# Performance work log

Hardware: AMD Instinct MI355X
Metric: run time of the kernel (lower is better)

Reference implementation:

```python
import jax, jax.numpy as jnp
import numpy as np

HEADS = 8
DIM_HEAD = 64
SCALE = DIM_HEAD ** -0.5


def setup_inputs() -> dict:
    key = jax.random.key(0)
    k1, k2, k3, k4 = jax.random.split(key, 4)
    dim = 512
    inner = HEADS * DIM_HEAD  # 512
    x = jax.random.normal(k1, (4, 2048, dim), dtype=jnp.float32)
    # torch nn.Linear weight layout: [out_features, in_features]
    w_qkv = jax.random.normal(k2, (inner * 3, dim), dtype=jnp.float32) * (dim ** -0.5)
    w_out = jax.random.normal(k3, (dim, inner), dtype=jnp.float32) * (inner ** -0.5)
    b_out = jax.random.normal(k4, (dim,), dtype=jnp.float32) * 0.01
    return {"x": x, "w_qkv": w_qkv, "w_out": w_out, "b_out": b_out}


def reference(x, w_qkv, w_out, b_out):
    b, n, _ = x.shape
    qkv = x @ w_qkv.T                                   # [b, n, 3*inner]
    q, k, v = jnp.split(qkv, 3, axis=-1)
    def to_heads(t):
        return t.reshape(b, n, HEADS, DIM_HEAD).transpose(0, 2, 1, 3)  # b h n d
    q, k, v = to_heads(q), to_heads(k), to_heads(v)
    dots = jnp.einsum('bhid,bhjd->bhij', q, k) * SCALE  # [b, h, n, n]
    attn = jax.nn.softmax(dots, axis=-1)
    out = jnp.einsum('bhij,bhjd->bhid', attn, v)        # [b, h, n, d]
    out = out.transpose(0, 2, 1, 3).reshape(b, n, HEADS * DIM_HEAD)
    return out @ w_out.T + b_out                        # [b, n, dim]
```

## Files before the change

kernel.cpp:

```cpp
#include <hip/hip_runtime.h>

typedef unsigned int u32;
typedef unsigned short u16;
typedef float f32x4 __attribute__((ext_vector_type(4)));
typedef u32 u32x4 __attribute__((ext_vector_type(4)));
typedef u32 u32x2 __attribute__((ext_vector_type(2)));

__device__ __forceinline__ u16 f2bf(float f) {
    u32 u = __builtin_bit_cast(u32, f);
    u = (u + 0x7FFFu + ((u >> 16) & 1u)) >> 16;
    return (u16)u;
}

__device__ __forceinline__ void mfma16(f32x4& d, const u32x4& a, const u32x4& b) {
    asm("v_mfma_f32_16x16x32_bf16 %0, %1, %2, %0" : "+v"(d) : "v"(a), "v"(b));
}

__device__ __forceinline__ float exp2a(float x) {
    float r;
    asm("v_exp_f32 %0, %1\n\ts_nop 1" : "=v"(r) : "v"(x));
    return r;
}
__device__ __forceinline__ u32 cvtpk(float lo, float hi) {
    u32 r;
    asm("v_cvt_pk_bf16_f32 %0, %1, %2" : "=v"(r) : "v"(lo), "v"(hi));
    return r;
}
__device__ __forceinline__ void gload_lds16(const u16* g, u16* l) {
    __builtin_amdgcn_global_load_lds(
        (const __attribute__((address_space(1))) u32*)g,
        (__attribute__((address_space(3))) u32*)l, 16, 0, 0);
}

__global__ __launch_bounds__(256) void cast3_kernel(
    const float* __restrict__ x, const float* __restrict__ wq,
    const float* __restrict__ wo, u16* __restrict__ xb,
    u16* __restrict__ wqb, u16* __restrict__ wob) {
    int bid = blockIdx.x;
    const float* src;
    u16* dst;
    int base;
    if (bid < 2048)      { src = x;  dst = xb;  base = bid * 2048; }
    else if (bid < 2432) { src = wq; dst = wqb; base = (bid - 2048) * 2048; }
    else                 { src = wo; dst = wob; base = (bid - 2432) * 2048; }
    int i = base + threadIdx.x * 8;
    float4 a = *(const float4*)(src + i);
    float4 b = *(const float4*)(src + i + 4);
    u32x4 r;
    r.x = (u32)f2bf(a.x) | ((u32)f2bf(a.y) << 16);
    r.y = (u32)f2bf(a.z) | ((u32)f2bf(a.w) << 16);
    r.z = (u32)f2bf(b.x) | ((u32)f2bf(b.y) << 16);
    r.w = (u32)f2bf(b.z) | ((u32)f2bf(b.w) << 16);
    *(u32x4*)(dst + i) = r;
}

template <int MODE>
__global__ __launch_bounds__(256) void gemm_bt(
    const u16* __restrict__ A, const u16* __restrict__ B, int K, int N,
    u16* __restrict__ qo, u16* __restrict__ ko, u16* __restrict__ vto,
    float* __restrict__ fo, const float* __restrict__ bias)
{
    __shared__ __align__(16) u16 Al[128 * 64];
    __shared__ __align__(16) u16 Bl[128 * 64];
    const int t = threadIdx.x;
    const int w = t >> 6, l = t & 63;
    const int wr = w >> 1, wc = w & 1;
    const int g = l >> 4, li = l & 15;
    const int m0 = blockIdx.x * 128, n0 = blockIdx.y * 128;

    const f32x4 z = {0.f, 0.f, 0.f, 0.f};
    f32x4 acc[4][4];
#pragma unroll
    for (int mi = 0; mi < 4; ++mi)
#pragma unroll
        for (int ni = 0; ni < 4; ++ni) acc[mi][ni] = z;

    int goff[4], ldst[4];
#pragma unroll
    for (int rnd = 0; rnd < 4; ++rnd) {
        int s = rnd * 256 + t;
        int p = s >> 3, cp = s & 7;
        int cg = cp ^ (p & 7);
        goff[rnd] = p * K + cg * 8;
        ldst[rnd] = s * 8;
    }

    for (int k0 = 0; k0 < K; k0 += 64) {
        __syncthreads();
#pragma unroll
        for (int rnd = 0; rnd < 4; ++rnd) {
            gload_lds16(A + (size_t)m0 * K + k0 + goff[rnd], &Al[ldst[rnd]]);
            gload_lds16(B + (size_t)n0 * K + k0 + goff[rnd], &Bl[ldst[rnd]]);
        }
        __syncthreads();
#pragma unroll
        for (int ks = 0; ks < 2; ++ks) {
            u32x4 af[4], bf[4];
#pragma unroll
            for (int mi = 0; mi < 4; ++mi)
                af[mi] = *(const u32x4*)&Al[(wr * 64 + mi * 16 + li) * 64
                                            + (((ks * 4 + g) ^ (li & 7)) * 8)];
#pragma unroll
            for (int ni = 0; ni < 4; ++ni)
                bf[ni] = *(const u32x4*)&Bl[(wc * 64 + ni * 16 + li) * 64
                                            + (((ks * 4 + g) ^ (li & 7)) * 8)];
#pragma unroll
            for (int mi = 0; mi < 4; ++mi)
#pragma unroll
                for (int ni = 0; ni < 4; ++ni) mfma16(acc[mi][ni], af[mi], bf[ni]);
        }
    }

#pragma unroll
    for (int mi = 0; mi < 4; ++mi) {
#pragma unroll
        for (int ni = 0; ni < 4; ++ni) {
            int o = n0 + wc * 64 + ni * 16 + li;
            int m_base = m0 + wr * 64 + mi * 16 + g * 4;
            if (MODE == 0) {
                int part = o >> 9, oi = o & 511;
                int h = oi >> 6, d = oi & 63;
                int bb = m_base >> 11, nn = m_base & 2047;
                if (part == 2) {
                    u32x2 pv;
                    pv.x = (u32)f2bf(acc[mi][ni][0]) | ((u32)f2bf(acc[mi][ni][1]) << 16);
                    pv.y = (u32)f2bf(acc[mi][ni][2]) | ((u32)f2bf(acc[mi][ni][3]) << 16);
                    *(u32x2*)(vto + ((size_t)(bb * 8 + h) * 64 + d) * 2048 + nn) = pv;
                } else {
                    u16* dst = (part == 0) ? qo : ko;
#pragma unroll
                    for (int r = 0; r < 4; ++r)
                        dst[((size_t)(bb * 8 + h) * 2048 + nn + r) * 64 + d] =
                            f2bf(acc[mi][ni][r]);
                }
            } else {
#pragma unroll
                for (int r = 0; r < 4; ++r)
                    fo[(size_t)(m_base + r) * N + o] = acc[mi][ni][r] + bias[o];
            }
        }
    }
}

__global__ __launch_bounds__(256) void attn_kernel(
    const u16* __restrict__ Q, const u16* __restrict__ Kg,
    const u16* __restrict__ VT, u16* __restrict__ O)
{
    __shared__ __align__(16) u16 Kl[64 * 64];
    __shared__ __align__(16) u16 Vl[64 * 64];
    const int t = threadIdx.x;
    const int w = t >> 6, l = t & 63;
    const int g = l >> 4, li = l & 15;
    const int pair = blockIdx.y;
    const int q0 = blockIdx.x * 128 + w * 32;
    const float CEXP = 0.18033688011112042f;

    u32x4 qf[2][2];
#pragma unroll
    for (int qb = 0; qb < 2; ++qb)
#pragma unroll
        for (int f = 0; f < 2; ++f)
            qf[qb][f] = *(const u32x4*)(Q + ((size_t)pair * 2048 + q0 + qb * 16 + li) * 64
                                          + f * 32 + g * 8);

    const f32x4 z = {0.f, 0.f, 0.f, 0.f};
    f32x4 oacc[2][4];
#pragma unroll
    for (int qb = 0; qb < 2; ++qb)
#pragma unroll
        for (int dc = 0; dc < 4; ++dc) oacc[qb][dc] = z;
    float m_r[2] = {-1e30f, -1e30f};
    float l_r[2] = {0.f, 0.f};

    for (int kt = 0; kt < 32; ++kt) {
        __syncthreads();
#pragma unroll
        for (int i = 0; i < 2; ++i) {
            int s = i * 256 + t;
            int p = s >> 3, cp = s & 7;
            int cg = (cp ^ (p & 7)) * 8;
            int kr = (p & 0x23) | ((p & 0x0C) << 1) | ((p & 0x10) >> 2);
            u32x4 kv = *(const u32x4*)(Kg + ((size_t)pair * 2048 + kt * 64 + kr) * 64 + cg);
            u32x4 vv = *(const u32x4*)(VT + ((size_t)pair * 64 + p) * 2048 + kt * 64 + cg);
            *(u32x4*)&Kl[p * 64 + cp * 8] = kv;
            *(u32x4*)&Vl[p * 64 + cp * 8] = vv;
        }
        __syncthreads();

        f32x4 st[2][4];
#pragma unroll
        for (int qb = 0; qb < 2; ++qb)
#pragma unroll
            for (int kc = 0; kc < 4; ++kc) st[qb][kc] = z;
#pragma unroll
        for (int kc = 0; kc < 4; ++kc)
#pragma unroll
            for (int f = 0; f < 2; ++f) {
                u32x4 kf = *(const u32x4*)&Kl[(kc * 16 + li) * 64
                                              + (((4 * f + g) ^ (li & 7)) * 8)];
                mfma16(st[0][kc], kf, qf[0][f]);
                mfma16(st[1][kc], kf, qf[1][f]);
            }

        u32x4 pb[2][2];
#pragma unroll
        for (int qb = 0; qb < 2; ++qb) {
            float a0 = fmaxf(fmaxf(st[qb][0][0], st[qb][0][1]), fmaxf(st[qb][0][2], st[qb][0][3]));
            float a1 = fmaxf(fmaxf(st[qb][1][0], st[qb][1][1]), fmaxf(st[qb][1][2], st[qb][1][3]));
            float a2 = fmaxf(fmaxf(st[qb][2][0], st[qb][2][1]), fmaxf(st[qb][2][2], st[qb][2][3]));
            float a3 = fmaxf(fmaxf(st[qb][3][0], st[qb][3][1]), fmaxf(st[qb][3][2], st[qb][3][3]));
            float tmax = fmaxf(fmaxf(a0, a1), fmaxf(a2, a3)) * CEXP;
            if (__any(tmax - m_r[qb] > 8.0f)) {
                float m4 = tmax;
                m4 = fmaxf(m4, __shfl_xor(m4, 16));
                m4 = fmaxf(m4, __shfl_xor(m4, 32));
                float mn = fmaxf(m_r[qb], m4);
                float alpha = exp2a(m_r[qb] - mn);
                m_r[qb] = mn;
                l_r[qb] *= alpha;
#pragma unroll
                for (int dc = 0; dc < 4; ++dc) oacc[qb][dc] *= alpha;
            }
            float nm = -m_r[qb];
            float ls0 = 0.f, ls1 = 0.f;
#pragma unroll
            for (int kc = 0; kc < 4; ++kc) {
#pragma unroll
                for (int r = 0; r < 4; ++r) {
                    float pv = exp2a(__builtin_fmaf(st[qb][kc][r], CEXP, nm));
                    st[qb][kc][r] = pv;
                    if (r & 1) ls1 += pv; else ls0 += pv;
                }
            }
            l_r[qb] += ls0 + ls1;
#pragma unroll
            for (int f = 0; f < 2; ++f) {
                u32x4 pk;
                pk.x = cvtpk(st[qb][2 * f][0], st[qb][2 * f][1]);
                pk.y = cvtpk(st[qb][2 * f][2], st[qb][2 * f][3]);
                pk.z = cvtpk(st[qb][2 * f + 1][0], st[qb][2 * f + 1][1]);
                pk.w = cvtpk(st[qb][2 * f + 1][2], st[qb][2 * f + 1][3]);
                pb[qb][f] = pk;
            }
        }

#pragma unroll
        for (int dc = 0; dc < 4; ++dc)
#pragma unroll
            for (int f = 0; f < 2; ++f) {
                u32x4 vf = *(const u32x4*)&Vl[(dc * 16 + li) * 64
                                              + (((4 * f + g) ^ (li & 7)) * 8)];
                mfma16(oacc[0][dc], vf, pb[0][f]);
                mfma16(oacc[1][dc], vf, pb[1][f]);
            }
    }

    const int bb = pair >> 3, h = pair & 7;
#pragma unroll
    for (int qb = 0; qb < 2; ++qb) {
        float ls = l_r[qb];
        ls += __shfl_xor(ls, 16);
        ls += __shfl_xor(ls, 32);
        float inv = 1.f / ls;
        u16* orow = O + ((size_t)bb * 2048 + q0 + qb * 16 + li) * 512 + h * 64;
#pragma unroll
        for (int dc = 0; dc < 4; ++dc) {
            u32x2 pv;
            pv.x = cvtpk(oacc[qb][dc][0] * inv, oacc[qb][dc][1] * inv);
            pv.y = cvtpk(oacc[qb][dc][2] * inv, oacc[qb][dc][3] * inv);
            *(u32x2*)(orow + dc * 16 + 4 * g) = pv;
        }
    }
}

extern "C" void kernel_launch(void* const* d_in, const int* in_sizes, int n_in,
                              void* d_out, int out_size, void* d_ws, size_t ws_size,
                              hipStream_t stream) {
    const float* x     = (const float*)d_in[0];
    const float* w_qkv = (const float*)d_in[1];
    const float* w_out = (const float*)d_in[2];
    const float* b_out = (const float*)d_in[3];
    float* out = (float*)d_out;

    char* ws = (char*)d_ws;
    u16* xb = (u16*)(ws + 0);
    u16* o  = (u16*)(ws + 0);
    u16* wq = (u16*)(ws + 8388608);
    u16* wo = (u16*)(ws + 9961472);
    u16* q  = (u16*)(ws + 10485760);
    u16* kk = (u16*)(ws + 18874368);
    u16* vt = (u16*)(ws + 27262976);

    cast3_kernel<<<2560, 256, 0, stream>>>(x, w_qkv, w_out, xb, wq, wo);

    gemm_bt<0><<<dim3(64, 12), 256, 0, stream>>>(xb, wq, 512, 1536,
                                                 q, kk, vt, nullptr, nullptr);
    attn_kernel<<<dim3(16, 32), 256, 0, stream>>>(q, kk, vt, o);

    gemm_bt<1><<<dim3(64, 4), 256, 0, stream>>>(o, wo, 512, 512,
                                                nullptr, nullptr, nullptr, out, b_out);
}
```

Baseline: 100.1 us.

## Load 128-key tiles via direct global-to-LDS loads and halve barrier count

The attention loop now stages two 64-key K/V sub-tiles per iteration (128 keys) into a doubled LDS buffer, cutting the number of __syncthreads pairs from 32 to 16. Global loads go through a gload_lds16 helper that writes straight into LDS, skipping the VGPR round trip, and the address offsets are precomputed outside the loop. The cost is double the LDS footprint (32KB per block), which can lower occupancy. Loads still are not overlapped with compute because a barrier follows them.

```diff
diff --git a/kernel.cpp b/kernel.cpp
--- a/kernel.cpp
+++ b/kernel.cpp
@@ -146,8 +146,8 @@
     const u16* __restrict__ Q, const u16* __restrict__ Kg,
     const u16* __restrict__ VT, u16* __restrict__ O)
 {
-    __shared__ __align__(16) u16 Kl[64 * 64];
-    __shared__ __align__(16) u16 Vl[64 * 64];
+    __shared__ __align__(16) u16 Kl[2 * 64 * 64];
+    __shared__ __align__(16) u16 Vl[2 * 64 * 64];
     const int t = threadIdx.x;
     const int w = t >> 6, l = t & 63;
     const int g = l >> 4, li = l & 15;
@@ -172,87 +172,102 @@
     float m_r[2] = {-1e30f, -1e30f};
     float l_r[2] = {0.f, 0.f};
 
-    for (int kt = 0; kt < 32; ++kt) {
+    int koff[4], voff[4], ldo[4];
+#pragma unroll
+    for (int i = 0; i < 4; ++i) {
+        int s = i * 256 + t;
+        int sub = s >> 9, sp = s & 511;
+        int p = sp >> 3, cp = sp & 7;
+        int cg = (cp ^ (p & 7)) * 8;
+        int kr = (p & 0x23) | ((p & 0x0C) << 1) | ((p & 0x10) >> 2);
+        koff[i] = (sub * 64 + kr) * 64 + cg;
+        voff[i] = p * 2048 + sub * 64 + cg;
+        ldo[i] = s * 8;
+    }
+    const u16* kbase = Kg + (size_t)pair * 2048 * 64;
+    const u16* vbase = VT + (size_t)pair * 64 * 2048;
+
+    for (int kt = 0; kt < 16; ++kt) {
         __syncthreads();
 #pragma unroll
-        for (int i = 0; i < 2; ++i) {
-            int s = i * 256 + t;
-            int p = s >> 3, cp = s & 7;
-            int cg = (cp ^ (p & 7)) * 8;
-            int kr = (p & 0x23) | ((p & 0x0C) << 1) | ((p & 0x10) >> 2);
-            u32x4 kv = *(const u32x4*)(Kg + ((size_t)pair * 2048 + kt * 64 + kr) * 64 + cg);
-            u32x4 vv = *(const u32x4*)(VT + ((size_t)pair * 64 + p) * 2048 + kt * 64 + cg);
-            *(u32x4*)&Kl[p * 64 + cp * 8] = kv;
-            *(u32x4*)&Vl[p * 64 + cp * 8] = vv;
+        for (int i = 0; i < 4; ++i) {
+            gload_lds16(kbase + (size_t)kt * 8192 + koff[i], &Kl[ldo[i]]);
+            gload_lds16(vbase + (size_t)kt * 128 + voff[i], &Vl[ldo[i]]);
         }
         __syncthreads();
 
-        f32x4 st[2][4];
-#pragma unroll
-        for (int qb = 0; qb < 2; ++qb)
-#pragma unroll
-            for (int kc = 0; kc < 4; ++kc) st[qb][kc] = z;
-#pragma unroll
-        for (int kc = 0; kc < 4; ++kc)
-#pragma unroll
-            for (int f = 0; f < 2; ++f) {
-                u32x4 kf = *(const u32x4*)&Kl[(kc * 16 + li) * 64
-                                              + (((4 * f + g) ^ (li & 7)) * 8)];
-                mfma16(st[0][kc], kf, qf[0][f]);
-                mfma16(st[1][kc], kf, qf[1][f]);
+#pragma unroll
+        for (int sub = 0; sub < 2; ++sub) {
+            const u16* kl = &Kl[sub * 4096];
+            const u16* vl = &Vl[sub * 4096];
+
+            f32x4 st[2][4];
+#pragma unroll
+            for (int qb = 0; qb < 2; ++qb)
+#pragma unroll
+                for (int kc = 0; kc < 4; ++kc) st[qb][kc] = z;
+#pragma unroll
+            for (int kc = 0; kc < 4; ++kc)
+#pragma unroll
+                for (int f = 0; f < 2; ++f) {
+                    u32x4 kf = *(const u32x4*)&kl[(kc * 16 + li) * 64
+                                                  + (((4 * f + g) ^ (li & 7)) * 8)];
+                    mfma16(st[0][kc], kf, qf[0][f]);
+                    mfma16(st[1][kc], kf, qf[1][f]);
+                }
+
+            u32x4 pb[2][2];
+#pragma unroll
+            for (int qb = 0; qb < 2; ++qb) {
+                float a0 = fmaxf(fmaxf(st[qb][0][0], st[qb][0][1]), fmaxf(st[qb][0][2], st[qb][0][3]));
+                float a1 = fmaxf(fmaxf(st[qb][1][0], st[qb][1][1]), fmaxf(st[qb][1][2], st[qb][1][3]));
+                float a2 = fmaxf(fmaxf(st[qb][2][0], st[qb][2][1]), fmaxf(st[qb][2][2], st[qb][2][3]));
+                float a3 = fmaxf(fmaxf(st[qb][3][0], st[qb][3][1]), fmaxf(st[qb][3][2], st[qb][3][3]));
+                float tmax = fmaxf(fmaxf(a0, a1), fmaxf(a2, a3)) * CEXP;
+                if (__any(tmax - m_r[qb] > 8.0f)) {
+                    float m4 = tmax;
+                    m4 = fmaxf(m4, __shfl_xor(m4, 16));
+                    m4 = fmaxf(m4, __shfl_xor(m4, 32));
+                    float mn = fmaxf(m_r[qb], m4);
+                    float alpha = exp2a(m_r[qb] - mn);
+                    m_r[qb] = mn;
+                    l_r[qb] *= alpha;
+#pragma unroll
+                    for (int dc = 0; dc < 4; ++dc) oacc[qb][dc] *= alpha;
+                }
+                float nm = -m_r[qb];
+                float ls0 = 0.f, ls1 = 0.f;
+#pragma unroll
+                for (int kc = 0; kc < 4; ++kc) {
+#pragma unroll
+                    for (int r = 0; r < 4; ++r) {
+                        float pv = exp2a(__builtin_fmaf(st[qb][kc][r], CEXP, nm));
+                        st[qb][kc][r] = pv;
+                        if (r & 1) ls1 += pv; else ls0 += pv;
+                    }
+                }
+                l_r[qb] += ls0 + ls1;
+#pragma unroll
+                for (int f = 0; f < 2; ++f) {
+                    u32x4 pk;
+                    pk.x = cvtpk(st[qb][2 * f][0], st[qb][2 * f][1]);
+                    pk.y = cvtpk(st[qb][2 * f][2], st[qb][2 * f][3]);
+                    pk.z = cvtpk(st[qb][2 * f + 1][0], st[qb][2 * f + 1][1]);
+                    pk.w = cvtpk(st[qb][2 * f + 1][2], st[qb][2 * f + 1][3]);
+                    pb[qb][f] = pk;
+                }
             }
 
-        u32x4 pb[2][2];
-#pragma unroll
-        for (int qb = 0; qb < 2; ++qb) {
-            float a0 = fmaxf(fmaxf(st[qb][0][0], st[qb][0][1]), fmaxf(st[qb][0][2], st[qb][0][3]));
-            float a1 = fmaxf(fmaxf(st[qb][1][0], st[qb][1][1]), fmaxf(st[qb][1][2], st[qb][1][3]));
-            float a2 = fmaxf(fmaxf(st[qb][2][0], st[qb][2][1]), fmaxf(st[qb][2][2], st[qb][2][3]));
-            float a3 = fmaxf(fmaxf(st[qb][3][0], st[qb][3][1]), fmaxf(st[qb][3][2], st[qb][3][3]));
-            float tmax = fmaxf(fmaxf(a0, a1), fmaxf(a2, a3)) * CEXP;
-            if (__any(tmax - m_r[qb] > 8.0f)) {
-                float m4 = tmax;
-                m4 = fmaxf(m4, __shfl_xor(m4, 16));
-                m4 = fmaxf(m4, __shfl_xor(m4, 32));
-                float mn = fmaxf(m_r[qb], m4);
-                float alpha = exp2a(m_r[qb] - mn);
-                m_r[qb] = mn;
-                l_r[qb] *= alpha;
-#pragma unroll
-                for (int dc = 0; dc < 4; ++dc) oacc[qb][dc] *= alpha;
-            }
-            float nm = -m_r[qb];
-            float ls0 = 0.f, ls1 = 0.f;
-#pragma unroll
-            for (int kc = 0; kc < 4; ++kc) {
-#pragma unroll
-                for (int r = 0; r < 4; ++r) {
-                    float pv = exp2a(__builtin_fmaf(st[qb][kc][r], CEXP, nm));
-                    st[qb][kc][r] = pv;
-                    if (r & 1) ls1 += pv; else ls0 += pv;
-                }
-            }
-            l_r[qb] += ls0 + ls1;
-#pragma unroll
-            for (int f = 0; f < 2; ++f) {
-                u32x4 pk;
-                pk.x = cvtpk(st[qb][2 * f][0], st[qb][2 * f][1]);
-                pk.y = cvtpk(st[qb][2 * f][2], st[qb][2 * f][3]);
-                pk.z = cvtpk(st[qb][2 * f + 1][0], st[qb][2 * f + 1][1]);
-                pk.w = cvtpk(st[qb][2 * f + 1][2], st[qb][2 * f + 1][3]);
-                pb[qb][f] = pk;
-            }
-        }
-
-#pragma unroll
-        for (int dc = 0; dc < 4; ++dc)
-#pragma unroll
-            for (int f = 0; f < 2; ++f) {
-                u32x4 vf = *(const u32x4*)&Vl[(dc * 16 + li) * 64
-                                              + (((4 * f + g) ^ (li & 7)) * 8)];
-                mfma16(oacc[0][dc], vf, pb[0][f]);
-                mfma16(oacc[1][dc], vf, pb[1][f]);
-            }
+#pragma unroll
+            for (int dc = 0; dc < 4; ++dc)
+#pragma unroll
+                for (int f = 0; f < 2; ++f) {
+                    u32x4 vf = *(const u32x4*)&vl[(dc * 16 + li) * 64
+                                                  + (((4 * f + g) ^ (li & 7)) * 8)];
+                    mfma16(oacc[0][dc], vf, pb[0][f]);
+                    mfma16(oacc[1][dc], vf, pb[1][f]);
+                }
+        }
     }
 
     const int bb = pair >> 3, h = pair & 7;
```

Measured after the change: 98.57 us. No clear change (-1.5%).
